# Kernel optimization log

Measured on AMD Instinct MI355X. Metric: run time of the kernel, lower is better.

Reference implementation:

```python
import jax, jax.numpy as jnp
import numpy as np


def rosa_batch(bits):
    """Vectorized ROSA (suffix-automaton 'predict next symbol of longest previously
    seen suffix') for a batch of binary sequences.

    bits: [N, T] int32 in {0,1}. Returns [N, T] int32 in {-1, 0, 1}.

    Equivalent to the serial suffix-automaton: at step i, let L = max_{j<i}
    lcs(i, j) (longest common suffix of prefixes ending at i and j). If L == 0
    the answer is -1; otherwise let e = max{ j < i : lcs(i, j) == L } (most
    recent occurrence end, matching the automaton's last-endpos bookkeeping)
    and the answer is bits[e + 1]. lcs follows the standard recurrence
    lcs(i, j) = (x[i] == x[j]) * (lcs(i-1, j-1) + 1), computed with a scan
    over i carrying the length-T lcs row, vmapped implicitly over N.
    """
    N, T = bits.shape
    jpos = jnp.arange(T)

    def step(prev, it):
        i, xt = it  # i: scalar step index, xt: [N] current symbols
        # prev[:, j] = lcs(i-1, j); shift to get lcs(i-1, j-1)
        shifted = jnp.concatenate([jnp.zeros((N, 1), prev.dtype), prev[:, :-1]], axis=1)
        cur = jnp.where(bits == xt[:, None], shifted + 1, 0)  # [N, T] lcs(i, j)
        valid = jpos[None, :] < i
        cm = jnp.where(valid, cur, -1)
        L = cm.max(axis=1)  # [N] longest previously-seen suffix length
        # most recent j < i achieving the max
        e = jnp.where(valid & (cm == L[:, None]), jpos[None, :], -1).max(axis=1)
        nxt = jnp.take_along_axis(bits, jnp.clip(e + 1, 0, T - 1)[:, None], axis=1)[:, 0]
        y = jnp.where(L > 0, nxt, -1)
        return cur, y

    _, ys = jax.lax.scan(step, jnp.zeros((N, T), jnp.int32), (jnp.arange(T), bits.T))
    return ys.T


def rosa_bits_btc(bits_btc):
    """bits_btc: [B, T, C] -> idx [B, T, C]; ROSA runs along T per (b, c)."""
    B, T, C = bits_btc.shape
    seqs = bits_btc.transpose(0, 2, 1).reshape(B * C, T)
    return rosa_batch(seqs).reshape(B, C, T).transpose(0, 2, 1)


def setup_inputs() -> dict:
    key = jax.random.key(0)
    B, T, C = 4, 2048, 128
    x = jax.random.normal(key, (B, T, C), dtype=jnp.float32)
    emb0 = jnp.full((1, 1, C), -1e-5, dtype=jnp.float32)
    emb1 = jnp.full((1, 1, C), 1e-5, dtype=jnp.float32)
    return {"x": x, "emb0": emb0, "emb1": emb1}


def reference(x, emb0, emb1):
    bits = (x > 0).astype(jnp.int32)
    idx = rosa_bits_btc(bits)  # [B, T, C] in {-1, 0, 1}
    return jnp.where(idx == -1, jnp.zeros_like(x), jnp.where(idx == 1, emb1, emb0))
```

## Files before the change

### kernel.cpp

```cpp
#include <hip/hip_runtime.h>


#define TT 2048
#define CC 128
#define NW 64
#define NSEQ 512
#define SBITS_WORDS (NSEQ * NW)
#define RES_WORDS (NSEQ * TT)

__global__ void k_bits(const float* __restrict__ x, unsigned* __restrict__ sbits)
{
    const int b = blockIdx.x >> 6;
    const int w = blockIdx.x & 63;
    const int t = threadIdx.x;
    __shared__ unsigned char sbyt[32 * 132];

    #pragma unroll
    for (int r = 0; r < 16; ++r) {
        const int e  = t + (r << 8);
        const int ii = e >> 7;
        const int c  = e & 127;
        const float v = x[((size_t)(b * TT + (w << 5) + ii)) * CC + c];
        sbyt[ii * 132 + c] = (v > 0.0f) ? 1u : 0u;
    }
    __syncthreads();

    if (t < CC) {
        unsigned word = 0u;
        #pragma unroll
        for (int ii = 0; ii < 32; ++ii)
            word |= (unsigned)(sbyt[ii * 132 + t] & 1u) << ii;
        sbits[((b << 7) | t) * NW + w] = word;
    }
}

__global__ __launch_bounds__(256, 4) void k_dp2(
    const unsigned* __restrict__ sbits, unsigned* __restrict__ res)
{
    const int u = blockIdx.x;
    const int q = blockIdx.y;
    int k = 0;
    #pragma unroll
    for (int kk = 1; kk < 8; ++kk) if (u >= (kk * (kk + 1)) / 2) k = kk;
    const int chunk = u - (k * (k + 1)) / 2;
    const int D0 = 1 + (chunk << 8);

    const int tid  = threadIdx.x;
    const int lane = tid & 63;
    const int wv   = tid >> 6;
    const int g    = lane >> 3;
    const int lm   = lane & 7;
    const int wloc = (k << 3) + lm;
    const int kb   = k << 8;

    __shared__ unsigned pad[128];
    __shared__ unsigned wres[4][8][33];

    if (tid < 64) pad[tid] = 0u;
    else if (tid < 128) pad[tid] = sbits[q * NW + (tid - 64)];
    __syncthreads();

    const unsigned a = pad[64 + wloc];

    unsigned lmax[32];
    #pragma unroll
    for (int bb = 0; bb < 32; ++bb) lmax[bb] = 0u;

    for (int it = 0; it < 8; ++it) {
        const int d  = D0 + (it << 5) + (wv << 3) + g;
        const int dw = d >> 5;
        const int dr = d & 31;
        const unsigned dcode = (unsigned)(TT - d);

        const int s = wloc - dw;
        const unsigned em = (s > 0) ? 0xFFFFFFFFu
                          : ((s == 0) ? (0xFFFFFFFFu << dr) : 0u);

        const unsigned b0 = pad[64 + s];
        const unsigned b1 = pad[63 + s];
        const unsigned sh = dr ? ((b0 << dr) | (b1 >> (32 - dr))) : b0;
        const unsigned m = (~(a ^ sh)) & em;

        unsigned inc0 = 0u;
        if (lm == 0 && d < kb) {
            int w = (k << 3) - 1;
            while (w >= 0) {
                const int ss = w - dw;
                const unsigned emw = (ss > 0) ? 0xFFFFFFFFu
                                   : ((ss == 0) ? (0xFFFFFFFFu << dr) : 0u);
                const unsigned c0 = pad[64 + ss];
                const unsigned c1 = pad[63 + ss];
                const unsigned shw = dr ? ((c0 << dr) | (c1 >> (32 - dr))) : c0;
                const unsigned mw = (~(pad[64 + w] ^ shw)) & emw;
                const unsigned t2 = (mw == 0xFFFFFFFFu) ? 32u
                                  : (unsigned)__builtin_clz(~mw);
                inc0 += t2;
                if (t2 < 32u) break;
                --w;
            }
        }

        unsigned inc;
        const unsigned long long anyfull = __ballot(m == 0xFFFFFFFFu);
        if (anyfull == 0ULL) {
            const unsigned pm = __shfl_up(m, 1);
            const unsigned lead = (unsigned)__builtin_clz(~pm);
            inc = (lm == 0) ? inc0 : lead;
        } else {
            unsigned gg = (m == 0xFFFFFFFFu) ? 1u : 0u;
            unsigned cc = gg ? 32u : (unsigned)__builtin_clz(~m | 1u);
            #pragma unroll
            for (int st = 1; st < 8; st <<= 1) {
                const unsigned gp = __shfl_up(gg, st);
                const unsigned cp = __shfl_up(cc, st);
                if (lm >= st) { cc += gg ? cp : 0u; gg &= gp; }
            }
            const unsigned h0 = __shfl(inc0, lane & ~7);
            const unsigned outl = cc + (gg ? h0 : 0u);
            const unsigned po = __shfl_up(outl, 1);
            inc = (lm == 0) ? inc0 : po;
        }

        unsigned pkv = (inc << 11) | dcode;
        #pragma unroll
        for (int bb = 0; bb < 32; ++bb) {
            unsigned keep;
            asm("v_bfe_i32 %0, %3, %4, 1\n\t"
                "v_add_u32 %1, 0x800, %1\n\t"
                "v_bfi_b32 %1, %0, %1, %5\n\t"
                "v_max_u32 %2, %2, %1"
                : "=&v"(keep), "+v"(pkv), "+v"(lmax[bb])
                : "v"(m), "n"(bb), "v"(dcode));
        }
    }

    #pragma unroll
    for (int bb = 0; bb < 32; ++bb) {
        unsigned v = lmax[bb];
        v = max(v, (unsigned)__shfl_xor((int)v, 8));
        v = max(v, (unsigned)__shfl_xor((int)v, 16));
        v = max(v, (unsigned)__shfl_xor((int)v, 32));
        lmax[bb] = v;
    }
    if (lane < 8) {
        #pragma unroll
        for (int bb = 0; bb < 32; ++bb) wres[wv][lane][bb] = lmax[bb];
    }
    __syncthreads();

    {
        const int lw = tid >> 5, bb = tid & 31;
        const unsigned v = max(max(wres[0][lw][bb], wres[1][lw][bb]),
                               max(wres[2][lw][bb], wres[3][lw][bb]));
        if (v >> 11) {
            const int i = ((k << 3) + lw) * 32 + bb;
            atomicMax(&res[(size_t)q * TT + i], v);
        }
    }
}

__global__ void k_dec(const unsigned* __restrict__ sbits,
                      const unsigned* __restrict__ res,
                      const float* __restrict__ emb0,
                      const float* __restrict__ emb1,
                      float* __restrict__ out)
{
    const int b  = blockIdx.y;
    const int i0 = blockIdx.x << 4;
    const int t  = threadIdx.x;
    __shared__ float trans[16][CC + 4];

    const int c  = t >> 1;
    const int q8 = (t & 1) << 3;
    const unsigned* rp = res + ((size_t)((b << 7) | c) * TT) + i0 + q8;
    const unsigned* bw = sbits + ((size_t)((b << 7) | c)) * NW;
    const float e0 = emb0[c], e1 = emb1[c];

    #pragma unroll
    for (int jj = 0; jj < 8; ++jj) {
        const unsigned v = rp[jj];
        const int i = i0 + q8 + jj;
        float val = 0.0f;
        if (v >> 11) {
            const int d   = TT - (int)(v & 2047u);
            const int e1p = i - d + 1;
            val = ((bw[e1p >> 5] >> (e1p & 31)) & 1u) ? e1 : e0;
        }
        trans[q8 + jj][c] = val;
    }
    __syncthreads();

    const int ii = t >> 4;
    const int c0 = (t & 15) << 3;
    float4 w0 = *(const float4*)&trans[ii][c0];
    float4 w1 = *(const float4*)&trans[ii][c0 + 4];
    float* op = out + ((size_t)(b * TT + i0 + ii)) * CC + c0;
    *(float4*)op       = w0;
    *(float4*)(op + 4) = w1;
}

extern "C" void kernel_launch(void* const* d_in, const int* in_sizes, int n_in,
                              void* d_out, int out_size, void* d_ws, size_t ws_size,
                              hipStream_t stream)
{
    const float* x    = (const float*)d_in[0];
    const float* emb0 = (const float*)d_in[1];
    const float* emb1 = (const float*)d_in[2];
    float* out        = (float*)d_out;

    unsigned* sbits = (unsigned*)d_ws;
    unsigned* res   = (unsigned*)d_ws + SBITS_WORDS;

    hipMemsetAsync((void*)res, 0, (size_t)RES_WORDS * 4, stream);
    k_bits<<<dim3(4 * 64), dim3(256), 0, stream>>>(x, sbits);
    k_dp2<<<dim3(36, NSEQ), dim3(256), 0, stream>>>(sbits, res);
    k_dec<<<dim3(TT / 16, 4), dim3(256), 0, stream>>>(sbits, res, emb0, emb1, out);
}
```

Measured before the change: 192.6 us.

## Carry run lengths across diagonal steps instead of per-step carry-chain scans

Restructures the LCS diagonal kernel so each 8-lane group walks a contiguous range of diagonals and propagates the run length between word lanes through a single shuffle of the previous step's result. The per-step ballot and log-step prefix scan, along with the backward word walk, are replaced by a one-word lookback with a rare fallback loop. The grid becomes one dimension with one block per (k, sequence), heaviest k scheduled first, and launch bounds drop to 2 blocks per SIMD. This removes the cross-lane scan work but adds a pipelined warm-up of extra steps per block and may lower occupancy.

```diff
diff --git a/kernel.cpp b/kernel.cpp
--- a/kernel.cpp
+++ b/kernel.cpp
@@ -34,94 +34,92 @@
     }
 }
 
-__global__ __launch_bounds__(256, 4) void k_dp2(
+__global__ __launch_bounds__(256, 2) void k_dp3(
     const unsigned* __restrict__ sbits, unsigned* __restrict__ res)
 {
-    const int u = blockIdx.x;
-    const int q = blockIdx.y;
-    int k = 0;
-    #pragma unroll
-    for (int kk = 1; kk < 8; ++kk) if (u >= (kk * (kk + 1)) / 2) k = kk;
-    const int chunk = u - (k * (k + 1)) / 2;
-    const int D0 = 1 + (chunk << 8);
+    const int bx = blockIdx.x;
+    const int k  = 7 - (bx >> 9);
+    const int q  = bx & 511;
+    const int L  = (k << 3) + 8;
+    const int nsteps = L + 7;
 
     const int tid  = threadIdx.x;
     const int lane = tid & 63;
     const int wv   = tid >> 6;
     const int g    = lane >> 3;
     const int lm   = lane & 7;
-    const int wloc = (k << 3) + lm;
-    const int kb   = k << 8;
-
-    __shared__ unsigned pad[128];
+    const int st   = (wv << 3) | g;
+    const int wB   = k << 3;
+    const int wloc = wB + lm;
+    const int dbase = 1 + st * L - lm;
+
+    __shared__ unsigned pad[136];
     __shared__ unsigned wres[4][8][33];
 
     if (tid < 64) pad[tid] = 0u;
     else if (tid < 128) pad[tid] = sbits[q * NW + (tid - 64)];
-    __syncthreads();
-
-    const unsigned a = pad[64 + wloc];
+    else if (tid < 136) pad[tid] = 0u;
+    __syncthreads();
+
+    const unsigned a  = pad[64 + wloc];
+    const unsigned W1 = (k > 0) ? pad[64 + wB - 1] : 0u;
 
     unsigned lmax[32];
     #pragma unroll
     for (int bb = 0; bb < 32; ++bb) lmax[bb] = 0u;
 
-    for (int it = 0; it < 8; ++it) {
-        const int d  = D0 + (it << 5) + (wv << 3) + g;
+    unsigned run_prev = 0u;
+
+    for (int s = 0; s < nsteps; ++s) {
+        const int d  = dbase + s;
         const int dw = d >> 5;
         const int dr = d & 31;
-        const unsigned dcode = (unsigned)(TT - d);
-
-        const int s = wloc - dw;
-        const unsigned em = (s > 0) ? 0xFFFFFFFFu
-                          : ((s == 0) ? (0xFFFFFFFFu << dr) : 0u);
-
-        const unsigned b0 = pad[64 + s];
-        const unsigned b1 = pad[63 + s];
+        const unsigned dcode = (unsigned)(TT - d) & 2047u;
+
+        const int si = wloc - dw;
+        const unsigned b0 = pad[64 + si];
+        const unsigned b1 = pad[63 + si];
         const unsigned sh = dr ? ((b0 << dr) | (b1 >> (32 - dr))) : b0;
+        unsigned em = (si > 0) ? 0xFFFFFFFFu : ((si == 0) ? (0xFFFFFFFFu << dr) : 0u);
+        if (d < 1) em = 0u;
         const unsigned m = (~(a ^ sh)) & em;
 
+        const unsigned rin = (unsigned)__shfl_up((int)run_prev, 1, 64);
+
         unsigned inc0 = 0u;
-        if (lm == 0 && d < kb) {
-            int w = (k << 3) - 1;
-            while (w >= 0) {
-                const int ss = w - dw;
-                const unsigned emw = (ss > 0) ? 0xFFFFFFFFu
-                                   : ((ss == 0) ? (0xFFFFFFFFu << dr) : 0u);
-                const unsigned c0 = pad[64 + ss];
-                const unsigned c1 = pad[63 + ss];
-                const unsigned shw = dr ? ((c0 << dr) | (c1 >> (32 - dr))) : c0;
-                const unsigned mw = (~(pad[64 + w] ^ shw)) & emw;
-                const unsigned t2 = (mw == 0xFFFFFFFFu) ? 32u
-                                  : (unsigned)__builtin_clz(~mw);
-                inc0 += t2;
-                if (t2 < 32u) break;
-                --w;
+        if (k > 0) {
+            const int s1 = (wB - 1) - dw;
+            const unsigned c0 = pad[64 + s1];
+            const unsigned c1 = pad[63 + s1];
+            const unsigned sh1 = dr ? ((c0 << dr) | (c1 >> (32 - dr))) : c0;
+            const unsigned e1 = (s1 > 0) ? 0xFFFFFFFFu
+                              : ((s1 == 0) ? (0xFFFFFFFFu << dr) : 0u);
+            const unsigned m1 = (~(W1 ^ sh1)) & e1;
+            const unsigned t1 = (m1 == 0xFFFFFFFFu) ? 32u : (unsigned)__builtin_clz(~m1);
+            inc0 = t1;
+            if (__builtin_expect(
+                    __ballot((lm == 0) && (t1 == 32u)) != 0ULL, 0)) {
+                if ((lm == 0) && t1 == 32u) {
+                    for (int w = wB - 2; w >= 0; --w) {
+                        const int sw = w - dw;
+                        const unsigned u0 = pad[64 + sw];
+                        const unsigned u1 = pad[63 + sw];
+                        const unsigned shw = dr ? ((u0 << dr) | (u1 >> (32 - dr))) : u0;
+                        const unsigned ew = (sw > 0) ? 0xFFFFFFFFu
+                                          : ((sw == 0) ? (0xFFFFFFFFu << dr) : 0u);
+                        const unsigned mw = (~(pad[64 + w] ^ shw)) & ew;
+                        const unsigned tw = (mw == 0xFFFFFFFFu) ? 32u
+                                          : (unsigned)__builtin_clz(~mw);
+                        inc0 += tw;
+                        if (tw < 32u) break;
+                    }
+                }
             }
         }
 
-        unsigned inc;
-        const unsigned long long anyfull = __ballot(m == 0xFFFFFFFFu);
-        if (anyfull == 0ULL) {
-            const unsigned pm = __shfl_up(m, 1);
-            const unsigned lead = (unsigned)__builtin_clz(~pm);
-            inc = (lm == 0) ? inc0 : lead;
-        } else {
-            unsigned gg = (m == 0xFFFFFFFFu) ? 1u : 0u;
-            unsigned cc = gg ? 32u : (unsigned)__builtin_clz(~m | 1u);
-            #pragma unroll
-            for (int st = 1; st < 8; st <<= 1) {
-                const unsigned gp = __shfl_up(gg, st);
-                const unsigned cp = __shfl_up(cc, st);
-                if (lm >= st) { cc += gg ? cp : 0u; gg &= gp; }
-            }
-            const unsigned h0 = __shfl(inc0, lane & ~7);
-            const unsigned outl = cc + (gg ? h0 : 0u);
-            const unsigned po = __shfl_up(outl, 1);
-            inc = (lm == 0) ? inc0 : po;
-        }
-
-        unsigned pkv = (inc << 11) | dcode;
+        const unsigned run_in = (lm == 0) ? inc0 : rin;
+        unsigned pkv = (run_in << 11) | dcode;
+
         #pragma unroll
         for (int bb = 0; bb < 32; ++bb) {
             unsigned keep;
@@ -132,14 +130,15 @@
                 : "=&v"(keep), "+v"(pkv), "+v"(lmax[bb])
                 : "v"(m), "n"(bb), "v"(dcode));
         }
+        run_prev = pkv >> 11;
     }
 
     #pragma unroll
     for (int bb = 0; bb < 32; ++bb) {
         unsigned v = lmax[bb];
-        v = max(v, (unsigned)__shfl_xor((int)v, 8));
-        v = max(v, (unsigned)__shfl_xor((int)v, 16));
-        v = max(v, (unsigned)__shfl_xor((int)v, 32));
+        v = max(v, (unsigned)__shfl_xor((int)v, 8, 64));
+        v = max(v, (unsigned)__shfl_xor((int)v, 16, 64));
+        v = max(v, (unsigned)__shfl_xor((int)v, 32, 64));
         lmax[bb] = v;
     }
     if (lane < 8) {
@@ -153,7 +152,7 @@
         const unsigned v = max(max(wres[0][lw][bb], wres[1][lw][bb]),
                                max(wres[2][lw][bb], wres[3][lw][bb]));
         if (v >> 11) {
-            const int i = ((k << 3) + lw) * 32 + bb;
+            const int i = ((wB + lw) << 5) + bb;
             atomicMax(&res[(size_t)q * TT + i], v);
         }
     }
@@ -213,6 +212,6 @@
 
     hipMemsetAsync((void*)res, 0, (size_t)RES_WORDS * 4, stream);
     k_bits<<<dim3(4 * 64), dim3(256), 0, stream>>>(x, sbits);
-    k_dp2<<<dim3(36, NSEQ), dim3(256), 0, stream>>>(sbits, res);
+    k_dp3<<<dim3(4096), dim3(256), 0, stream>>>(sbits, res);
     k_dec<<<dim3(TT / 16, 4), dim3(256), 0, stream>>>(sbits, res, emb0, emb1, out);
 }
```

Result: slower. 209.9 us (+9.0%).

## Precompute per-diagonal seed carries in parallel and simplify carry propagation

Applied to the files above, without the earlier changes.

Before the main loop, all 256 threads compute the cross-block carry (matching-run length entering the 8-word window) for their own diagonal and store it in shared memory. Previously only lane 0 of each 8-lane group computed it serially inside each iteration, which caused divergence. The ballot-driven prefix-scan path over full match words is replaced by a cheap shfl_up/clz path. A rare per-lane serial fallback walks back through full words when the previous word matched completely. The iteration loop is also fully unrolled, which adds a shared buffer and some register pressure.

```diff
diff --git a/kernel.cpp b/kernel.cpp
--- a/kernel.cpp
+++ b/kernel.cpp
@@ -50,22 +50,48 @@
     const int wv   = tid >> 6;
     const int g    = lane >> 3;
     const int lm   = lane & 7;
-    const int wloc = (k << 3) + lm;
+    const int wB   = k << 3;
+    const int wloc = wB + lm;
     const int kb   = k << 8;
 
     __shared__ unsigned pad[128];
+    __shared__ unsigned seedl[256];
     __shared__ unsigned wres[4][8][33];
 
     if (tid < 64) pad[tid] = 0u;
     else if (tid < 128) pad[tid] = sbits[q * NW + (tid - 64)];
     __syncthreads();
 
+    {
+        const int d = D0 + tid;
+        unsigned acc = 0u;
+        if (d < kb) {
+            const int dw = d >> 5, dr = d & 31;
+            for (int w = wB - 1; w >= 0; --w) {
+                const int sw = w - dw;
+                const unsigned u0 = pad[64 + sw];
+                const unsigned u1 = pad[63 + sw];
+                const unsigned shw = dr ? ((u0 << dr) | (u1 >> (32 - dr))) : u0;
+                const unsigned ew = (sw > 0) ? 0xFFFFFFFFu
+                                  : ((sw == 0) ? (0xFFFFFFFFu << dr) : 0u);
+                const unsigned mw = (~(pad[64 + w] ^ shw)) & ew;
+                const unsigned t2 = (mw == 0xFFFFFFFFu) ? 32u
+                                  : (unsigned)__builtin_clz(~mw);
+                acc += t2;
+                if (t2 < 32u) break;
+            }
+        }
+        seedl[tid] = acc;
+    }
+    __syncthreads();
+
     const unsigned a = pad[64 + wloc];
 
     unsigned lmax[32];
     #pragma unroll
     for (int bb = 0; bb < 32; ++bb) lmax[bb] = 0u;
 
+    #pragma unroll
     for (int it = 0; it < 8; ++it) {
         const int d  = D0 + (it << 5) + (wv << 3) + g;
         const int dw = d >> 5;
@@ -73,52 +99,39 @@
         const unsigned dcode = (unsigned)(TT - d);
 
         const int s = wloc - dw;
-        const unsigned em = (s > 0) ? 0xFFFFFFFFu
-                          : ((s == 0) ? (0xFFFFFFFFu << dr) : 0u);
-
         const unsigned b0 = pad[64 + s];
         const unsigned b1 = pad[63 + s];
         const unsigned sh = dr ? ((b0 << dr) | (b1 >> (32 - dr))) : b0;
+        const unsigned em = (s > 0) ? 0xFFFFFFFFu
+                          : ((s == 0) ? (0xFFFFFFFFu << dr) : 0u);
         const unsigned m = (~(a ^ sh)) & em;
 
-        unsigned inc0 = 0u;
-        if (lm == 0 && d < kb) {
-            int w = (k << 3) - 1;
-            while (w >= 0) {
-                const int ss = w - dw;
-                const unsigned emw = (ss > 0) ? 0xFFFFFFFFu
-                                   : ((ss == 0) ? (0xFFFFFFFFu << dr) : 0u);
-                const unsigned c0 = pad[64 + ss];
-                const unsigned c1 = pad[63 + ss];
-                const unsigned shw = dr ? ((c0 << dr) | (c1 >> (32 - dr))) : c0;
-                const unsigned mw = (~(pad[64 + w] ^ shw)) & emw;
-                const unsigned t2 = (mw == 0xFFFFFFFFu) ? 32u
-                                  : (unsigned)__builtin_clz(~mw);
-                inc0 += t2;
-                if (t2 < 32u) break;
-                --w;
+        const unsigned seedv = seedl[(it << 5) + (wv << 3) + g];
+        const unsigned pm = (unsigned)__shfl_up((int)m, 1, 64);
+        const unsigned lead = (unsigned)__builtin_clz(~pm | 1u);
+        unsigned inc = (lm == 0) ? seedv : lead;
+
+        if (__builtin_expect(
+                __ballot((lm > 0) && (pm == 0xFFFFFFFFu)) != 0ULL, 0)) {
+            if ((lm > 0) && (pm == 0xFFFFFFFFu)) {
+                unsigned acc = 0u;
+                int w;
+                for (w = wloc - 1; w >= wB; --w) {
+                    const int sw = w - dw;
+                    const unsigned u0 = pad[64 + sw];
+                    const unsigned u1 = pad[63 + sw];
+                    const unsigned shw = dr ? ((u0 << dr) | (u1 >> (32 - dr))) : u0;
+                    const unsigned ew = (sw > 0) ? 0xFFFFFFFFu
+                                      : ((sw == 0) ? (0xFFFFFFFFu << dr) : 0u);
+                    const unsigned mw = (~(pad[64 + w] ^ shw)) & ew;
+                    const unsigned t2 = (mw == 0xFFFFFFFFu) ? 32u
+                                      : (unsigned)__builtin_clz(~mw);
+                    acc += t2;
+                    if (t2 < 32u) break;
+                }
+                if (w < wB) acc += seedv;
+                inc = acc;
             }
-        }
-
-        unsigned inc;
-        const unsigned long long anyfull = __ballot(m == 0xFFFFFFFFu);
-        if (anyfull == 0ULL) {
-            const unsigned pm = __shfl_up(m, 1);
-            const unsigned lead = (unsigned)__builtin_clz(~pm);
-            inc = (lm == 0) ? inc0 : lead;
-        } else {
-            unsigned gg = (m == 0xFFFFFFFFu) ? 1u : 0u;
-            unsigned cc = gg ? 32u : (unsigned)__builtin_clz(~m | 1u);
-            #pragma unroll
-            for (int st = 1; st < 8; st <<= 1) {
-                const unsigned gp = __shfl_up(gg, st);
-                const unsigned cp = __shfl_up(cc, st);
-                if (lm >= st) { cc += gg ? cp : 0u; gg &= gp; }
-            }
-            const unsigned h0 = __shfl(inc0, lane & ~7);
-            const unsigned outl = cc + (gg ? h0 : 0u);
-            const unsigned po = __shfl_up(outl, 1);
-            inc = (lm == 0) ? inc0 : po;
         }
 
         unsigned pkv = (inc << 11) | dcode;
@@ -137,9 +150,9 @@
     #pragma unroll
     for (int bb = 0; bb < 32; ++bb) {
         unsigned v = lmax[bb];
-        v = max(v, (unsigned)__shfl_xor((int)v, 8));
-        v = max(v, (unsigned)__shfl_xor((int)v, 16));
-        v = max(v, (unsigned)__shfl_xor((int)v, 32));
+        v = max(v, (unsigned)__shfl_xor((int)v, 8, 64));
+        v = max(v, (unsigned)__shfl_xor((int)v, 16, 64));
+        v = max(v, (unsigned)__shfl_xor((int)v, 32, 64));
         lmax[bb] = v;
     }
     if (lane < 8) {
@@ -153,7 +166,7 @@
         const unsigned v = max(max(wres[0][lw][bb], wres[1][lw][bb]),
                                max(wres[2][lw][bb], wres[3][lw][bb]));
         if (v >> 11) {
-            const int i = ((k << 3) + lw) * 32 + bb;
+            const int i = ((wB + lw) << 5) + bb;
             atomicMax(&res[(size_t)q * TT + i], v);
         }
     }
```

Measured after the change: 179.6 us. 1.07x faster.
